# Performance work log

Measured on AMD Instinct MI355X. Metric: run time of the kernel, lower is better.

Reference implementation:

```python
import jax, jax.numpy as jnp
import numpy as np

NUM_EXPERTS = 8
HIDDEN = 2048
FFN = 1376
CAPACITY_FACTOR = 1.25
SCORE_SCALE = 1.0


def setup_inputs() -> dict:
    key = jax.random.key(0)
    k = jax.random.split(key, 6)
    T = 8192
    x = jax.random.normal(k[0], (T, HIDDEN), dtype=jnp.float32)
    topK_indices = jax.random.randint(k[1], (T,), 0, NUM_EXPERTS, dtype=jnp.int64)
    topK_scores = jax.random.uniform(k[2], (T,), dtype=jnp.float32)
    s = 1.0 / np.sqrt(HIDDEN)
    w_gate = jax.random.normal(k[3], (NUM_EXPERTS, HIDDEN, FFN), dtype=jnp.float32) * s
    w_up = jax.random.normal(k[4], (NUM_EXPERTS, HIDDEN, FFN), dtype=jnp.float32) * s
    w_down = jax.random.normal(k[5], (NUM_EXPERTS, FFN, HIDDEN), dtype=jnp.float32) * (1.0 / np.sqrt(FFN))
    return {"x": x, "topK_indices": topK_indices, "topK_scores": topK_scores,
            "w_gate": w_gate, "w_up": w_up, "w_down": w_down}


def reference(x, topK_indices, topK_scores, w_gate, w_up, w_down):
    T, D = x.shape
    E = w_gate.shape[0]
    capacity = int(CAPACITY_FACTOR * T / E)  # static (depends only on shapes)
    # position of each token within its assigned expert (deterministic drop:
    # keep the first `capacity` tokens in sequence order per expert)
    oh = jax.nn.one_hot(topK_indices, E, dtype=jnp.int32)          # [T,E]
    rank = jnp.take_along_axis(jnp.cumsum(oh, axis=0) - 1,
                               topK_indices[:, None].astype(jnp.int32), axis=1)[:, 0]
    keep = rank < capacity                                          # [T]
    # dispatch into per-expert capacity buffers; dropped tokens go to dummy slot
    slot = jnp.where(keep, topK_indices.astype(jnp.int32) * capacity + rank, E * capacity)
    buf = jnp.zeros((E * capacity + 1, D), x.dtype)
    buf = buf.at[slot].set(jnp.where(keep[:, None], x, jnp.zeros_like(x)))
    xe = buf[:E * capacity].reshape(E, capacity, D)                 # [E,C,D]
    # per-expert SwiGLU MLP as grouped GEMMs
    h = jax.nn.silu(jnp.einsum('ecd,edf->ecf', xe, w_gate)) * jnp.einsum('ecd,edf->ecf', xe, w_up)
    out = jnp.einsum('ecf,efd->ecd', h, w_down).reshape(E * capacity, D)
    out = jnp.concatenate([out, jnp.zeros((1, D), out.dtype)], axis=0)
    # combine: dropped tokens -> zero (dropped_padding='zero'), gate-score fusion
    y = out[slot] * keep[:, None].astype(out.dtype)
    y = y * (topK_scores[:, None] * SCORE_SCALE)
    return y
```

## Files before the change

### kernel.cpp

```cpp
#include <hip/hip_runtime.h>
#include <hip/hip_bf16.h>
#include <cstdint>
#include <cstddef>

#define NTOK 8192
#define DH   2048
#define DF   1376
#define NE   8
#define CAP  1280

typedef __bf16 bf16x8 __attribute__((ext_vector_type(8)));
typedef float  f32x4  __attribute__((ext_vector_type(4)));

#define BARRIER() asm volatile("s_barrier" ::: "memory")
#define WAITV(n)  asm volatile("s_waitcnt vmcnt(" #n ")" ::: "memory")
#define LGKM(n)   asm volatile("s_waitcnt lgkmcnt(" #n ")" ::: "memory")
#define SCHED0()  __builtin_amdgcn_sched_barrier(0)
#define SETPRIO(n) __builtin_amdgcn_s_setprio(n)

__device__ __forceinline__ uint32_t pk2(float a, float b) {
  float2 f; f.x = a; f.y = b;
  union { __hip_bfloat162 h; uint32_t u; } cv;
  cv.h = __float22bfloat162_rn(f);
  return cv.u;
}
__device__ __forceinline__ ushort bf16bits(float a) {
  return (ushort)(pk2(a, 0.f) & 0xFFFFu);
}
__device__ __forceinline__ void gload16(const ushort* g, ushort* l) {
  __builtin_amdgcn_global_load_lds(
      (const __attribute__((address_space(1))) uint32_t*)(const void*)g,
      (__attribute__((address_space(3))) uint32_t*)(void*)l,
      16, 0, 0);
}

__device__ __forceinline__ void rp_src(int o, int& row, int& ko) {
  int p = o >> 7;
  int g = ((o >> 4) & 7) ^ (p & 7);
  row = p * 2 + (g >> 2);
  ko  = (g & 3) * 8;
}
__device__ __forceinline__ int rp_off(int row, int l4) {
  return ((row >> 1) << 7) + (((((row & 1) << 2) + l4) ^ ((row >> 1) & 7)) << 4);
}

__global__ void routing_kernel(const int* __restrict__ idx, int* __restrict__ tok_slot,
                               int* __restrict__ tok_keep) {
  __shared__ int cnt[256][NE];
  const int t = threadIdx.x;
  for (int s = t; s < NE * CAP; s += 256) tok_slot[s] = -1;
  unsigned long long cA = 0ull, cB = 0ull;
  const int per = NTOK / 256, base = t * per;
  for (int i = 0; i < per; ++i) {
    int e = idx[base + i];
    unsigned long long inc = 1ull << ((e & 3) * 16);
    if (e < 4) cA += inc; else cB += inc;
  }
#pragma unroll
  for (int e = 0; e < 4; ++e) cnt[t][e]     = (int)((cA >> (e * 16)) & 0xFFFF);
#pragma unroll
  for (int e = 0; e < 4; ++e) cnt[t][4 + e] = (int)((cB >> (e * 16)) & 0xFFFF);
  __syncthreads();
  if (t < NE) {
    int run = 0;
    for (int i = 0; i < 256; ++i) { int c = cnt[i][t]; cnt[i][t] = run; run += c; }
  }
  __syncthreads();
  cA = 0ull; cB = 0ull;
#pragma unroll
  for (int e = 0; e < 4; ++e) cA |= (unsigned long long)(cnt[t][e] & 0xFFFF) << (e * 16);
#pragma unroll
  for (int e = 0; e < 4; ++e) cB |= (unsigned long long)(cnt[t][4 + e] & 0xFFFF) << (e * 16);
  for (int i = 0; i < per; ++i) {
    int token = base + i;
    int e = idx[token];
    int sh = (e & 3) * 16;
    int r = (int)(((e < 4 ? cA : cB) >> sh) & 0xFFFF);
    unsigned long long inc = 1ull << sh;
    if (e < 4) cA += inc; else cB += inc;
    bool keep = (r < CAP);
    tok_keep[token] = keep ? 1 : 0;
    if (keep) tok_slot[e * CAP + r] = token;
  }
}

__global__ void xconv_zero(const float* __restrict__ x, const int* __restrict__ keep,
                           ushort* __restrict__ xb, float* __restrict__ y) {
  const int row = blockIdx.x;
  const int c = threadIdx.x * 8;
  const size_t off = (size_t)row * DH + c;
  float4 a = *(const float4*)(x + off);
  float4 b = *(const float4*)(x + off + 4);
  uint4 p = { pk2(a.x, a.y), pk2(a.z, a.w), pk2(b.x, b.y), pk2(b.z, b.w) };
  *(uint4*)(xb + off) = p;
  if (!keep[row]) {
    float4 z = {0.f, 0.f, 0.f, 0.f};
    *(float4*)(y + off) = z;
    *(float4*)(y + off + 4) = z;
  }
}

__global__ __launch_bounds__(256) void transpose_all(
    const float* __restrict__ wg, const float* __restrict__ wu, const float* __restrict__ wd,
    ushort* __restrict__ wgt, ushort* __restrict__ wut, ushort* __restrict__ wdt) {
  const int z = blockIdx.z;
  const float* in; ushort* out; int K, N, eidx;
  if (z < 8)       { in = wg; out = wgt; K = DH; N = DF; eidx = z; }
  else if (z < 16) { in = wu; out = wut; K = DH; N = DF; eidx = z - 8; }
  else             { in = wd; out = wdt; K = DF; N = DH; eidx = z - 16; }
  const int n0 = blockIdx.x * 64, k0 = blockIdx.y * 64;
  if (n0 >= N || k0 >= K) return;
  __shared__ ushort T[64][72];
  const int tid = threadIdx.x;
  const size_t eoff_in  = (size_t)eidx * K * N;
  const size_t eoff_out = (size_t)eidx * N * K;
  const int kr = tid >> 4;
  const int nc = (tid & 15) * 4;
#pragma unroll
  for (int it = 0; it < 4; ++it) {
    int k = k0 + kr + it * 16;
    int n = n0 + nc;
    float4 v = {0.f, 0.f, 0.f, 0.f};
    if (k < K && n + 4 <= N) v = *(const float4*)(in + eoff_in + (size_t)k * N + n);
    T[nc + 0][kr + it * 16] = bf16bits(v.x);
    T[nc + 1][kr + it * 16] = bf16bits(v.y);
    T[nc + 2][kr + it * 16] = bf16bits(v.z);
    T[nc + 3][kr + it * 16] = bf16bits(v.w);
  }
  __syncthreads();
  const int nr = tid >> 2;
  const int kc = tid & 3;
#pragma unroll
  for (int it = 0; it < 2; ++it) {
    int kloc = kc * 16 + it * 8;
    int n = n0 + nr, k = k0 + kloc;
    if (n < N && k + 8 <= K)
      *(uint4*)(out + eoff_out + (size_t)n * K + k) = *(const uint4*)&T[nr][kloc];
  }
}

#define GU_READ(SET, RB) { \
  char* Ab_  = sm + (RB) * 16384; \
  char* Bgb_ = sm + 65536 + (RB) * 8192; \
  char* Bub_ = sm + 98304 + (RB) * 8192; \
  _Pragma("unroll") for (int i_ = 0; i_ < 4; ++i_) aR##SET[i_]  = *(const bf16x8*)(Ab_ + aoff[i_]); \
  _Pragma("unroll") for (int j_ = 0; j_ < 4; ++j_) bgR##SET[j_] = *(const bf16x8*)(Bgb_ + boff[j_]); \
  _Pragma("unroll") for (int j_ = 0; j_ < 4; ++j_) buR##SET[j_] = *(const bf16x8*)(Bub_ + boff[j_]); \
}
#define GU_MFMA(SET) { \
  _Pragma("unroll") for (int j_ = 0; j_ < 4; ++j_) \
    _Pragma("unroll") for (int i_ = 0; i_ < 4; ++i_) \
      accG[i_][j_] = __builtin_amdgcn_mfma_f32_16x16x32_bf16(aR##SET[i_], bgR##SET[j_], accG[i_][j_], 0, 0, 0); \
  _Pragma("unroll") for (int j_ = 0; j_ < 4; ++j_) \
    _Pragma("unroll") for (int i_ = 0; i_ < 4; ++i_) \
      accU[i_][j_] = __builtin_amdgcn_mfma_f32_16x16x32_bf16(aR##SET[i_], buR##SET[j_], accU[i_][j_], 0, 0, 0); \
}
#define GU_BODY(T, CUR, NXT) { \
  const int t_ = (T); \
  if (t_ + 3 < NT) { \
    const int kk_ = (t_ + 3) * 32; const int w_ = (t_ + 3) & 3; \
    gload16(srcA[0] + kk_, (ushort*)(sm + w_ * 16384 + dstw)); \
    gload16(srcA[1] + kk_, (ushort*)(sm + w_ * 16384 + 8192 + dstw)); \
    gload16(srcBg + kk_, (ushort*)(sm + 65536 + w_ * 8192 + dstw)); \
    gload16(srcBu + kk_, (ushort*)(sm + 98304 + w_ * 8192 + dstw)); \
  } \
  if (t_ + 1 < NT) { GU_READ(NXT, (t_ + 1) & 3); LGKM(12); } else { LGKM(0); } \
  SCHED0(); SETPRIO(1); \
  GU_MFMA(CUR); \
  SETPRIO(0); SCHED0(); \
  if (t_ + 3 < NT) { WAITV(4); } else if (t_ + 2 < NT) { WAITV(0); } \
  BARRIER(); \
}

__global__ __launch_bounds__(512, 2) void gemm_gateup3(
    const ushort* __restrict__ xb, const ushort* __restrict__ wgt,
    const ushort* __restrict__ wut, const int* __restrict__ tok_slot,
    ushort* __restrict__ h)
{
  __shared__ __align__(16) char sm[131072];
  const int tid = threadIdx.x, lane = tid & 63, wid = tid >> 6;
  const int wr = wid >> 1, wc = wid & 1;
  const int l15 = lane & 15, l4 = lane >> 4;

  int wgid = (blockIdx.x & 7) * 55 + (blockIdx.x >> 3);
  const int e = wgid / 55;
  const int rem = wgid - e * 55;
  const int mt = rem / 11, nt = rem - (rem / 11) * 11;
  const int n0 = nt * 128;

  const ushort* srcA[2]; const ushort* srcBg; const ushort* srcBu;
#pragma unroll
  for (int c = 0; c < 2; ++c) {
    int o = c * 8192 + wid * 1024 + lane * 16;
    int row, ko; rp_src(o, row, ko);
    int tk = tok_slot[e * CAP + mt * 256 + row];
    if (tk < 0) tk = 0;
    srcA[c] = xb + (size_t)tk * DH + ko;
  }
  {
    int o = wid * 1024 + lane * 16;
    int row, ko; rp_src(o, row, ko);
    int n = n0 + row; if (n > DF - 1) n = DF - 1;
    srcBg = wgt + ((size_t)e * DF + n) * DH + ko;
    srcBu = wut + ((size_t)e * DF + n) * DH + ko;
  }
  int aoff[4], boff[4];
#pragma unroll
  for (int i = 0; i < 4; ++i) aoff[i] = rp_off(wr * 64 + i * 16 + l15, l4);
#pragma unroll
  for (int j = 0; j < 4; ++j) boff[j] = rp_off(wc * 64 + j * 16 + l15, l4);
  const int dstw = wid * 1024;

  f32x4 accG[4][4], accU[4][4];
#pragma unroll
  for (int i = 0; i < 4; ++i)
#pragma unroll
    for (int j = 0; j < 4; ++j) {
      accG[i][j] = (f32x4){0.f, 0.f, 0.f, 0.f};
      accU[i][j] = (f32x4){0.f, 0.f, 0.f, 0.f};
    }

  const int NT = DH / 32;
#pragma unroll
  for (int t0 = 0; t0 < 3; ++t0) {
    int kk = t0 * 32;
    gload16(srcA[0] + kk, (ushort*)(sm + t0 * 16384 + dstw));
    gload16(srcA[1] + kk, (ushort*)(sm + t0 * 16384 + 8192 + dstw));
    gload16(srcBg   + kk, (ushort*)(sm + 65536 + t0 * 8192 + dstw));
    gload16(srcBu   + kk, (ushort*)(sm + 98304 + t0 * 8192 + dstw));
  }
  WAITV(4);
  BARRIER();

  bf16x8 aR0[4], bgR0[4], buR0[4], aR1[4], bgR1[4], buR1[4];
  GU_READ(0, 0);

  for (int t = 0; t < NT; t += 2) {
    GU_BODY(t, 0, 1);
    GU_BODY(t + 1, 1, 0);
  }

  const size_t rowbase = (size_t)(e * CAP + mt * 256 + wr * 64);
#pragma unroll
  for (int j = 0; j < 4; ++j) {
    int col = n0 + wc * 64 + j * 16 + l15;
    if (col < DF) {
#pragma unroll
      for (int i = 0; i < 4; ++i)
#pragma unroll
        for (int r2 = 0; r2 < 4; ++r2) {
          size_t row = rowbase + i * 16 + l4 * 4 + r2;
          float gv = accG[i][j][r2], uv = accU[i][j][r2];
          h[row * DF + col] = bf16bits(gv / (1.f + __expf(-gv)) * uv);
        }
    }
  }
}

#define DN_READ(SET, RB) { \
  char* Ab_ = sm + (RB) * 16384; \
  char* Bb_ = sm + 65536 + (RB) * 8192; \
  _Pragma("unroll") for (int i_ = 0; i_ < 4; ++i_) aR##SET[i_] = *(const bf16x8*)(Ab_ + aoff[i_]); \
  _Pragma("unroll") for (int j_ = 0; j_ < 4; ++j_) bR##SET[j_] = *(const bf16x8*)(Bb_ + boff[j_]); \
}
#define DN_MFMA(SET) { \
  _Pragma("unroll") for (int j_ = 0; j_ < 4; ++j_) \
    _Pragma("unroll") for (int i_ = 0; i_ < 4; ++i_) \
      acc[i_][j_] = __builtin_amdgcn_mfma_f32_16x16x32_bf16(aR##SET[i_], bR##SET[j_], acc[i_][j_], 0, 0, 0); \
}
#define DN_BODY(T, CUR, NXT) { \
  const int t_ = (T); \
  if (t_ + 3 < NT) { \
    const int kk_ = (t_ + 3) * 32; const int w_ = (t_ + 3) & 3; \
    gload16(srcA[0] + kk_, (ushort*)(sm + w_ * 16384 + dstw)); \
    gload16(srcA[1] + kk_, (ushort*)(sm + w_ * 16384 + 8192 + dstw)); \
    gload16(srcB + kk_, (ushort*)(sm + 65536 + w_ * 8192 + dstw)); \
  } \
  if (t_ + 1 < NT) { DN_READ(NXT, (t_ + 1) & 3); LGKM(8); } else { LGKM(0); } \
  SCHED0(); SETPRIO(1); \
  DN_MFMA(CUR); \
  SETPRIO(0); SCHED0(); \
  if (t_ + 3 < NT) { WAITV(3); } else if (t_ + 2 < NT) { WAITV(0); } \
  BARRIER(); \
}

__global__ __launch_bounds__(512, 2) void gemm_down3(
    const ushort* __restrict__ h, const ushort* __restrict__ wdt,
    const int* __restrict__ tok_slot, const float* __restrict__ scores,
    float* __restrict__ y)
{
  __shared__ __align__(16) char sm[100352];
  int* tokc = (int*)(sm + 98304);
  float* scc = (float*)(sm + 99328);
  const int tid = threadIdx.x, lane = tid & 63, wid = tid >> 6;
  const int wr = wid >> 1, wc = wid & 1;
  const int l15 = lane & 15, l4 = lane >> 4;

  int wgid = (blockIdx.x & 7) * 80 + (blockIdx.x >> 3);
  const int e = wgid / 80;
  const int rem = wgid - e * 80;
  const int mt = rem / 16, nt = rem & 15;
  const int n0 = nt * 128;

  if (tid < 256) {
    int tk = tok_slot[e * CAP + mt * 256 + tid];
    tokc[tid] = tk;
    scc[tid] = (tk >= 0) ? scores[tk] : 0.f;
  }
  __syncthreads();

  const size_t hrow0 = (size_t)(e * CAP + mt * 256);
  const ushort* srcA[2]; const ushort* srcB;
#pragma unroll
  for (int c = 0; c < 2; ++c) {
    int o = c * 8192 + wid * 1024 + lane * 16;
    int row, ko; rp_src(o, row, ko);
    srcA[c] = h + (hrow0 + row) * DF + ko;
  }
  {
    int o = wid * 1024 + lane * 16;
    int row, ko; rp_src(o, row, ko);
    srcB = wdt + ((size_t)e * DH + n0 + row) * DF + ko;
  }
  int aoff[4], boff[4];
#pragma unroll
  for (int i = 0; i < 4; ++i) aoff[i] = rp_off(wr * 64 + i * 16 + l15, l4);
#pragma unroll
  for (int j = 0; j < 4; ++j) boff[j] = rp_off(wc * 64 + j * 16 + l15, l4);
  const int dstw = wid * 1024;

  f32x4 acc[4][4];
#pragma unroll
  for (int i = 0; i < 4; ++i)
#pragma unroll
    for (int j = 0; j < 4; ++j) acc[i][j] = (f32x4){0.f, 0.f, 0.f, 0.f};

  const int NT = DF / 32;
#pragma unroll
  for (int t0 = 0; t0 < 3; ++t0) {
    int kk = t0 * 32;
    gload16(srcA[0] + kk, (ushort*)(sm + t0 * 16384 + dstw));
    gload16(srcA[1] + kk, (ushort*)(sm + t0 * 16384 + 8192 + dstw));
    gload16(srcB    + kk, (ushort*)(sm + 65536 + t0 * 8192 + dstw));
  }
  WAITV(3);
  BARRIER();

  bf16x8 aR0[4], bR0[4], aR1[4], bR1[4];
  DN_READ(0, 0);

  for (int t = 0; t < NT - 1; t += 2) {
    DN_BODY(t, 0, 1);
    DN_BODY(t + 1, 1, 0);
  }
  DN_BODY(NT - 1, 0, 1);

  int tkr[4][4]; float sr[4][4];
#pragma unroll
  for (int i = 0; i < 4; ++i)
#pragma unroll
    for (int r = 0; r < 4; ++r) {
      int rl = wr * 64 + i * 16 + l4 * 4 + r;
      tkr[i][r] = tokc[rl];
      sr[i][r]  = scc[rl];
    }
#pragma unroll
  for (int j = 0; j < 4; ++j) {
    int col = n0 + wc * 64 + j * 16 + l15;
#pragma unroll
    for (int i = 0; i < 4; ++i)
#pragma unroll
      for (int r = 0; r < 4; ++r)
        if (tkr[i][r] >= 0)
          y[(size_t)tkr[i][r] * DH + col] = acc[i][j][r] * sr[i][r];
  }
}

extern "C" void kernel_launch(void* const* d_in, const int* in_sizes, int n_in,
                              void* d_out, int out_size, void* d_ws, size_t ws_size,
                              hipStream_t stream) {
  const float* x   = (const float*)d_in[0];
  const int*   idx = (const int*)d_in[1];
  const float* sc  = (const float*)d_in[2];
  const float* wg  = (const float*)d_in[3];
  const float* wu  = (const float*)d_in[4];
  const float* wd  = (const float*)d_in[5];
  float* y = (float*)d_out;

  const size_t OFF_KEEP = 40960;
  const size_t OFF_H    = 73728;
  const size_t SZ_H     = (size_t)NE * CAP * DF * 2;
  const size_t OFF_XB   = OFF_H + SZ_H;
  const size_t SZ_XB    = (size_t)NTOK * DH * 2;
  const size_t OFF_WGT  = OFF_XB + SZ_XB;
  const size_t SZ_W     = (size_t)NE * DH * DF * 2;
  const size_t OFF_WUT  = OFF_WGT + SZ_W;
  const size_t OFF_WDT  = OFF_WUT + SZ_W;

  int* tok_slot = (int*)d_ws;
  int* tok_keep = (int*)((char*)d_ws + OFF_KEEP);
  ushort* hbuf = (ushort*)((char*)d_ws + OFF_H);
  ushort* xb   = (ushort*)((char*)d_ws + OFF_XB);
  ushort* wgt  = (ushort*)((char*)d_ws + OFF_WGT);
  ushort* wut  = (ushort*)((char*)d_ws + OFF_WUT);
  ushort* wdt  = (ushort*)((char*)d_ws + OFF_WDT);

  hipLaunchKernelGGL(routing_kernel, dim3(1), dim3(256), 0, stream, idx, tok_slot, tok_keep);
  hipLaunchKernelGGL(xconv_zero, dim3(NTOK), dim3(256), 0, stream, x, tok_keep, xb, y);
  hipLaunchKernelGGL(transpose_all, dim3(32, 32, 24), dim3(256), 0, stream,
                     wg, wu, wd, wgt, wut, wdt);
  hipLaunchKernelGGL(gemm_gateup3, dim3(440), dim3(512), 0, stream,
                     xb, wgt, wut, tok_slot, hbuf);
  hipLaunchKernelGGL(gemm_down3, dim3(640), dim3(512), 0, stream,
                     hbuf, wdt, tok_slot, sc, y);
}
```

Baseline: 333.4 us.

## Halve GEMM M-tile to 128 and raise occupancy to four blocks per CU

Both grouped GEMM kernels shrink the M tile from 256 to 128 rows, cut the LDS ring from four stages to three, and drop the register double-buffered fragment prefetch in favour of a simple load-then-wait loop. Launch bounds move from 2 to 4 blocks per CU and the grid doubles, so more waves can hide latency through occupancy rather than software pipelining. The trade-off is lower arithmetic intensity per block (B tiles are reloaded twice as often) and full lgkmcnt(0) stalls before each MFMA group.

```diff
diff --git a/kernel.cpp b/kernel.cpp
--- a/kernel.cpp
+++ b/kernel.cpp
@@ -14,7 +14,7 @@
 
 #define BARRIER() asm volatile("s_barrier" ::: "memory")
 #define WAITV(n)  asm volatile("s_waitcnt vmcnt(" #n ")" ::: "memory")
-#define LGKM(n)   asm volatile("s_waitcnt lgkmcnt(" #n ")" ::: "memory")
+#define LGKM0()   asm volatile("s_waitcnt lgkmcnt(0)" ::: "memory")
 #define SCHED0()  __builtin_amdgcn_sched_barrier(0)
 #define SETPRIO(n) __builtin_amdgcn_s_setprio(n)
 
@@ -139,81 +139,43 @@
   }
 }
 
-#define GU_READ(SET, RB) { \
-  char* Ab_  = sm + (RB) * 16384; \
-  char* Bgb_ = sm + 65536 + (RB) * 8192; \
-  char* Bub_ = sm + 98304 + (RB) * 8192; \
-  _Pragma("unroll") for (int i_ = 0; i_ < 4; ++i_) aR##SET[i_]  = *(const bf16x8*)(Ab_ + aoff[i_]); \
-  _Pragma("unroll") for (int j_ = 0; j_ < 4; ++j_) bgR##SET[j_] = *(const bf16x8*)(Bgb_ + boff[j_]); \
-  _Pragma("unroll") for (int j_ = 0; j_ < 4; ++j_) buR##SET[j_] = *(const bf16x8*)(Bub_ + boff[j_]); \
-}
-#define GU_MFMA(SET) { \
-  _Pragma("unroll") for (int j_ = 0; j_ < 4; ++j_) \
-    _Pragma("unroll") for (int i_ = 0; i_ < 4; ++i_) \
-      accG[i_][j_] = __builtin_amdgcn_mfma_f32_16x16x32_bf16(aR##SET[i_], bgR##SET[j_], accG[i_][j_], 0, 0, 0); \
-  _Pragma("unroll") for (int j_ = 0; j_ < 4; ++j_) \
-    _Pragma("unroll") for (int i_ = 0; i_ < 4; ++i_) \
-      accU[i_][j_] = __builtin_amdgcn_mfma_f32_16x16x32_bf16(aR##SET[i_], buR##SET[j_], accU[i_][j_], 0, 0, 0); \
-}
-#define GU_BODY(T, CUR, NXT) { \
-  const int t_ = (T); \
-  if (t_ + 3 < NT) { \
-    const int kk_ = (t_ + 3) * 32; const int w_ = (t_ + 3) & 3; \
-    gload16(srcA[0] + kk_, (ushort*)(sm + w_ * 16384 + dstw)); \
-    gload16(srcA[1] + kk_, (ushort*)(sm + w_ * 16384 + 8192 + dstw)); \
-    gload16(srcBg + kk_, (ushort*)(sm + 65536 + w_ * 8192 + dstw)); \
-    gload16(srcBu + kk_, (ushort*)(sm + 98304 + w_ * 8192 + dstw)); \
-  } \
-  if (t_ + 1 < NT) { GU_READ(NXT, (t_ + 1) & 3); LGKM(12); } else { LGKM(0); } \
-  SCHED0(); SETPRIO(1); \
-  GU_MFMA(CUR); \
-  SETPRIO(0); SCHED0(); \
-  if (t_ + 3 < NT) { WAITV(4); } else if (t_ + 2 < NT) { WAITV(0); } \
-  BARRIER(); \
-}
-
-__global__ __launch_bounds__(512, 2) void gemm_gateup3(
+__global__ __launch_bounds__(512, 4) void gemm_gateup4(
     const ushort* __restrict__ xb, const ushort* __restrict__ wgt,
     const ushort* __restrict__ wut, const int* __restrict__ tok_slot,
     ushort* __restrict__ h)
 {
-  __shared__ __align__(16) char sm[131072];
+  __shared__ __align__(16) char sm[73728];
   const int tid = threadIdx.x, lane = tid & 63, wid = tid >> 6;
   const int wr = wid >> 1, wc = wid & 1;
   const int l15 = lane & 15, l4 = lane >> 4;
 
-  int wgid = (blockIdx.x & 7) * 55 + (blockIdx.x >> 3);
-  const int e = wgid / 55;
-  const int rem = wgid - e * 55;
-  const int mt = rem / 11, nt = rem - (rem / 11) * 11;
+  int wgid = (blockIdx.x & 7) * 110 + (blockIdx.x >> 3);
+  const int e = wgid / 110;
+  const int rem = wgid - e * 110;
+  const int mt = rem % 10, nt = rem / 10;
   const int n0 = nt * 128;
 
-  const ushort* srcA[2]; const ushort* srcBg; const ushort* srcBu;
-#pragma unroll
-  for (int c = 0; c < 2; ++c) {
-    int o = c * 8192 + wid * 1024 + lane * 16;
-    int row, ko; rp_src(o, row, ko);
-    int tk = tok_slot[e * CAP + mt * 256 + row];
-    if (tk < 0) tk = 0;
-    srcA[c] = xb + (size_t)tk * DH + ko;
-  }
+  const ushort* srcA; const ushort* srcBg; const ushort* srcBu;
   {
     int o = wid * 1024 + lane * 16;
     int row, ko; rp_src(o, row, ko);
+    int tk = tok_slot[e * CAP + mt * 128 + row];
+    if (tk < 0) tk = 0;
+    srcA = xb + (size_t)tk * DH + ko;
     int n = n0 + row; if (n > DF - 1) n = DF - 1;
     srcBg = wgt + ((size_t)e * DF + n) * DH + ko;
     srcBu = wut + ((size_t)e * DF + n) * DH + ko;
   }
-  int aoff[4], boff[4];
-#pragma unroll
-  for (int i = 0; i < 4; ++i) aoff[i] = rp_off(wr * 64 + i * 16 + l15, l4);
+  int aoff[2], boff[4];
+#pragma unroll
+  for (int i = 0; i < 2; ++i) aoff[i] = rp_off(wr * 32 + i * 16 + l15, l4);
 #pragma unroll
   for (int j = 0; j < 4; ++j) boff[j] = rp_off(wc * 64 + j * 16 + l15, l4);
   const int dstw = wid * 1024;
 
-  f32x4 accG[4][4], accU[4][4];
-#pragma unroll
-  for (int i = 0; i < 4; ++i)
+  f32x4 accG[2][4], accU[2][4];
+#pragma unroll
+  for (int i = 0; i < 2; ++i)
 #pragma unroll
     for (int j = 0; j < 4; ++j) {
       accG[i][j] = (f32x4){0.f, 0.f, 0.f, 0.f};
@@ -222,31 +184,61 @@
 
   const int NT = DH / 32;
 #pragma unroll
-  for (int t0 = 0; t0 < 3; ++t0) {
+  for (int t0 = 0; t0 < 2; ++t0) {
     int kk = t0 * 32;
-    gload16(srcA[0] + kk, (ushort*)(sm + t0 * 16384 + dstw));
-    gload16(srcA[1] + kk, (ushort*)(sm + t0 * 16384 + 8192 + dstw));
-    gload16(srcBg   + kk, (ushort*)(sm + 65536 + t0 * 8192 + dstw));
-    gload16(srcBu   + kk, (ushort*)(sm + 98304 + t0 * 8192 + dstw));
-  }
-  WAITV(4);
+    gload16(srcA  + kk, (ushort*)(sm + t0 * 8192 + dstw));
+    gload16(srcBg + kk, (ushort*)(sm + 24576 + t0 * 8192 + dstw));
+    gload16(srcBu + kk, (ushort*)(sm + 49152 + t0 * 8192 + dstw));
+  }
+  WAITV(3);
   BARRIER();
 
-  bf16x8 aR0[4], bgR0[4], buR0[4], aR1[4], bgR1[4], buR1[4];
-  GU_READ(0, 0);
-
-  for (int t = 0; t < NT; t += 2) {
-    GU_BODY(t, 0, 1);
-    GU_BODY(t + 1, 1, 0);
-  }
-
-  const size_t rowbase = (size_t)(e * CAP + mt * 256 + wr * 64);
+  int rb = 0, wb = 2;
+  for (int t = 0; t < NT; ++t) {
+    char* Ab  = sm + rb * 8192;
+    char* Bgb = sm + 24576 + rb * 8192;
+    char* Bub = sm + 49152 + rb * 8192;
+    if (t + 2 < NT) {
+      const int kk = (t + 2) * 32;
+      gload16(srcA  + kk, (ushort*)(sm + wb * 8192 + dstw));
+      gload16(srcBg + kk, (ushort*)(sm + 24576 + wb * 8192 + dstw));
+      gload16(srcBu + kk, (ushort*)(sm + 49152 + wb * 8192 + dstw));
+    }
+    bf16x8 a[2], b[4];
+#pragma unroll
+    for (int i = 0; i < 2; ++i) a[i] = *(const bf16x8*)(Ab + aoff[i]);
+#pragma unroll
+    for (int j = 0; j < 4; ++j) b[j] = *(const bf16x8*)(Bgb + boff[j]);
+    LGKM0(); SCHED0();
+    SETPRIO(1);
+#pragma unroll
+    for (int j = 0; j < 4; ++j)
+#pragma unroll
+      for (int i = 0; i < 2; ++i)
+        accG[i][j] = __builtin_amdgcn_mfma_f32_16x16x32_bf16(a[i], b[j], accG[i][j], 0, 0, 0);
+    SETPRIO(0); SCHED0();
+#pragma unroll
+    for (int j = 0; j < 4; ++j) b[j] = *(const bf16x8*)(Bub + boff[j]);
+    LGKM0(); SCHED0();
+    SETPRIO(1);
+#pragma unroll
+    for (int j = 0; j < 4; ++j)
+#pragma unroll
+      for (int i = 0; i < 2; ++i)
+        accU[i][j] = __builtin_amdgcn_mfma_f32_16x16x32_bf16(a[i], b[j], accU[i][j], 0, 0, 0);
+    SETPRIO(0); SCHED0();
+    if (t + 2 < NT) { WAITV(3); } else { WAITV(0); }
+    BARRIER();
+    rb = (rb == 2) ? 0 : rb + 1;
+    wb = (wb == 2) ? 0 : wb + 1;
+  }
+  const size_t rowbase = (size_t)(e * CAP + mt * 128 + wr * 32);
 #pragma unroll
   for (int j = 0; j < 4; ++j) {
     int col = n0 + wc * 64 + j * 16 + l15;
     if (col < DF) {
 #pragma unroll
-      for (int i = 0; i < 4; ++i)
+      for (int i = 0; i < 2; ++i)
 #pragma unroll
         for (int r2 = 0; r2 < 4; ++r2) {
           size_t row = rowbase + i * 16 + l4 * 4 + r2;
@@ -257,110 +249,95 @@
   }
 }
 
-#define DN_READ(SET, RB) { \
-  char* Ab_ = sm + (RB) * 16384; \
-  char* Bb_ = sm + 65536 + (RB) * 8192; \
-  _Pragma("unroll") for (int i_ = 0; i_ < 4; ++i_) aR##SET[i_] = *(const bf16x8*)(Ab_ + aoff[i_]); \
-  _Pragma("unroll") for (int j_ = 0; j_ < 4; ++j_) bR##SET[j_] = *(const bf16x8*)(Bb_ + boff[j_]); \
-}
-#define DN_MFMA(SET) { \
-  _Pragma("unroll") for (int j_ = 0; j_ < 4; ++j_) \
-    _Pragma("unroll") for (int i_ = 0; i_ < 4; ++i_) \
-      acc[i_][j_] = __builtin_amdgcn_mfma_f32_16x16x32_bf16(aR##SET[i_], bR##SET[j_], acc[i_][j_], 0, 0, 0); \
-}
-#define DN_BODY(T, CUR, NXT) { \
-  const int t_ = (T); \
-  if (t_ + 3 < NT) { \
-    const int kk_ = (t_ + 3) * 32; const int w_ = (t_ + 3) & 3; \
-    gload16(srcA[0] + kk_, (ushort*)(sm + w_ * 16384 + dstw)); \
-    gload16(srcA[1] + kk_, (ushort*)(sm + w_ * 16384 + 8192 + dstw)); \
-    gload16(srcB + kk_, (ushort*)(sm + 65536 + w_ * 8192 + dstw)); \
-  } \
-  if (t_ + 1 < NT) { DN_READ(NXT, (t_ + 1) & 3); LGKM(8); } else { LGKM(0); } \
-  SCHED0(); SETPRIO(1); \
-  DN_MFMA(CUR); \
-  SETPRIO(0); SCHED0(); \
-  if (t_ + 3 < NT) { WAITV(3); } else if (t_ + 2 < NT) { WAITV(0); } \
-  BARRIER(); \
-}
-
-__global__ __launch_bounds__(512, 2) void gemm_down3(
+__global__ __launch_bounds__(512, 4) void gemm_down4(
     const ushort* __restrict__ h, const ushort* __restrict__ wdt,
     const int* __restrict__ tok_slot, const float* __restrict__ scores,
     float* __restrict__ y)
 {
-  __shared__ __align__(16) char sm[100352];
-  int* tokc = (int*)(sm + 98304);
-  float* scc = (float*)(sm + 99328);
+  __shared__ __align__(16) char sm[50176];
+  int* tokc = (int*)(sm + 49152);
+  float* scc = (float*)(sm + 49664);
   const int tid = threadIdx.x, lane = tid & 63, wid = tid >> 6;
   const int wr = wid >> 1, wc = wid & 1;
   const int l15 = lane & 15, l4 = lane >> 4;
 
-  int wgid = (blockIdx.x & 7) * 80 + (blockIdx.x >> 3);
-  const int e = wgid / 80;
-  const int rem = wgid - e * 80;
-  const int mt = rem / 16, nt = rem & 15;
+  int wgid = (blockIdx.x & 7) * 160 + (blockIdx.x >> 3);
+  const int e = wgid / 160;
+  const int rem = wgid - e * 160;
+  const int mt = rem % 10, nt = rem / 10;
   const int n0 = nt * 128;
 
-  if (tid < 256) {
-    int tk = tok_slot[e * CAP + mt * 256 + tid];
+  if (tid < 128) {
+    int tk = tok_slot[e * CAP + mt * 128 + tid];
     tokc[tid] = tk;
     scc[tid] = (tk >= 0) ? scores[tk] : 0.f;
   }
   __syncthreads();
 
-  const size_t hrow0 = (size_t)(e * CAP + mt * 256);
-  const ushort* srcA[2]; const ushort* srcB;
-#pragma unroll
-  for (int c = 0; c < 2; ++c) {
-    int o = c * 8192 + wid * 1024 + lane * 16;
-    int row, ko; rp_src(o, row, ko);
-    srcA[c] = h + (hrow0 + row) * DF + ko;
-  }
+  const size_t hrow0 = (size_t)(e * CAP + mt * 128);
+  const ushort* srcA; const ushort* srcB;
   {
     int o = wid * 1024 + lane * 16;
     int row, ko; rp_src(o, row, ko);
+    srcA = h + (hrow0 + row) * DF + ko;
     srcB = wdt + ((size_t)e * DH + n0 + row) * DF + ko;
   }
-  int aoff[4], boff[4];
-#pragma unroll
-  for (int i = 0; i < 4; ++i) aoff[i] = rp_off(wr * 64 + i * 16 + l15, l4);
+  int aoff[2], boff[4];
+#pragma unroll
+  for (int i = 0; i < 2; ++i) aoff[i] = rp_off(wr * 32 + i * 16 + l15, l4);
 #pragma unroll
   for (int j = 0; j < 4; ++j) boff[j] = rp_off(wc * 64 + j * 16 + l15, l4);
   const int dstw = wid * 1024;
 
-  f32x4 acc[4][4];
-#pragma unroll
-  for (int i = 0; i < 4; ++i)
+  f32x4 acc[2][4];
+#pragma unroll
+  for (int i = 0; i < 2; ++i)
 #pragma unroll
     for (int j = 0; j < 4; ++j) acc[i][j] = (f32x4){0.f, 0.f, 0.f, 0.f};
 
   const int NT = DF / 32;
 #pragma unroll
-  for (int t0 = 0; t0 < 3; ++t0) {
+  for (int t0 = 0; t0 < 2; ++t0) {
     int kk = t0 * 32;
-    gload16(srcA[0] + kk, (ushort*)(sm + t0 * 16384 + dstw));
-    gload16(srcA[1] + kk, (ushort*)(sm + t0 * 16384 + 8192 + dstw));
-    gload16(srcB    + kk, (ushort*)(sm + 65536 + t0 * 8192 + dstw));
-  }
-  WAITV(3);
+    gload16(srcA + kk, (ushort*)(sm + t0 * 8192 + dstw));
+    gload16(srcB + kk, (ushort*)(sm + 24576 + t0 * 8192 + dstw));
+  }
+  WAITV(2);
   BARRIER();
 
-  bf16x8 aR0[4], bR0[4], aR1[4], bR1[4];
-  DN_READ(0, 0);
-
-  for (int t = 0; t < NT - 1; t += 2) {
-    DN_BODY(t, 0, 1);
-    DN_BODY(t + 1, 1, 0);
-  }
-  DN_BODY(NT - 1, 0, 1);
-
-  int tkr[4][4]; float sr[4][4];
-#pragma unroll
-  for (int i = 0; i < 4; ++i)
+  int rb = 0, wb = 2;
+  for (int t = 0; t < NT; ++t) {
+    char* Ab = sm + rb * 8192;
+    char* Bb = sm + 24576 + rb * 8192;
+    if (t + 2 < NT) {
+      const int kk = (t + 2) * 32;
+      gload16(srcA + kk, (ushort*)(sm + wb * 8192 + dstw));
+      gload16(srcB + kk, (ushort*)(sm + 24576 + wb * 8192 + dstw));
+    }
+    bf16x8 a[2], b[4];
+#pragma unroll
+    for (int i = 0; i < 2; ++i) a[i] = *(const bf16x8*)(Ab + aoff[i]);
+#pragma unroll
+    for (int j = 0; j < 4; ++j) b[j] = *(const bf16x8*)(Bb + boff[j]);
+    LGKM0(); SCHED0();
+    SETPRIO(1);
+#pragma unroll
+    for (int j = 0; j < 4; ++j)
+#pragma unroll
+      for (int i = 0; i < 2; ++i)
+        acc[i][j] = __builtin_amdgcn_mfma_f32_16x16x32_bf16(a[i], b[j], acc[i][j], 0, 0, 0);
+    SETPRIO(0); SCHED0();
+    if (t + 2 < NT) { WAITV(2); } else { WAITV(0); }
+    BARRIER();
+    rb = (rb == 2) ? 0 : rb + 1;
+    wb = (wb == 2) ? 0 : wb + 1;
+  }
+  int tkr[2][4]; float sr[2][4];
+#pragma unroll
+  for (int i = 0; i < 2; ++i)
 #pragma unroll
     for (int r = 0; r < 4; ++r) {
-      int rl = wr * 64 + i * 16 + l4 * 4 + r;
+      int rl = wr * 32 + i * 16 + l4 * 4 + r;
       tkr[i][r] = tokc[rl];
       sr[i][r]  = scc[rl];
     }
@@ -368,7 +345,7 @@
   for (int j = 0; j < 4; ++j) {
     int col = n0 + wc * 64 + j * 16 + l15;
 #pragma unroll
-    for (int i = 0; i < 4; ++i)
+    for (int i = 0; i < 2; ++i)
 #pragma unroll
       for (int r = 0; r < 4; ++r)
         if (tkr[i][r] >= 0)
@@ -409,8 +386,8 @@
   hipLaunchKernelGGL(xconv_zero, dim3(NTOK), dim3(256), 0, stream, x, tok_keep, xb, y);
   hipLaunchKernelGGL(transpose_all, dim3(32, 32, 24), dim3(256), 0, stream,
                      wg, wu, wd, wgt, wut, wdt);
-  hipLaunchKernelGGL(gemm_gateup3, dim3(440), dim3(512), 0, stream,
+  hipLaunchKernelGGL(gemm_gateup4, dim3(880), dim3(512), 0, stream,
                      xb, wgt, wut, tok_slot, hbuf);
-  hipLaunchKernelGGL(gemm_down3, dim3(640), dim3(512), 0, stream,
+  hipLaunchKernelGGL(gemm_down4, dim3(1280), dim3(512), 0, stream,
                      hbuf, wdt, tok_slot, sc, y);
 }
```

Measured after the change: 347.1 us. 4.1% more time.
